# Kernel tuning notes

Measured on AMD Instinct MI355X. Metric: run time of the kernel, lower is better.

## Reference

```python
import jax, jax.numpy as jnp
import numpy as np

N_QUBITS = 64
L = 128
K = 2
B = 4096
M_EVO = 5
A = N_QUBITS * 3 * M_EVO  # 960
E = 2 * (N_QUBITS - 1)    # 126 directed chain edges


def setup_inputs() -> dict:
    key = jax.random.key(0)
    ks = iter(jax.random.split(key, 32))

    def nrm(shape, s=0.05):
        return jax.random.normal(next(ks), shape, dtype=jnp.float32) * s

    # chain edges, both directions: (i,i+1) and (i+1,i)
    src = jnp.asarray(np.concatenate([np.arange(N_QUBITS - 1), np.arange(1, N_QUBITS)]), dtype=jnp.int32)
    tgt = jnp.asarray(np.concatenate([np.arange(1, N_QUBITS), np.arange(N_QUBITS - 1)]), dtype=jnp.int32)
    edge_attr = jnp.full((E, 1), 0.1, dtype=jnp.float32)

    return {
        "z0": jax.random.normal(next(ks), (B, L), dtype=jnp.float32),
        "src": src,
        "tgt": tgt,
        "edge_attr": edge_attr,
        "phiE_W1": nrm((K, 2 * L + 1, L)), "phiE_b1": jnp.zeros((K, L), jnp.float32),
        "phiE_W2": nrm((K, L, L)),          "phiE_b2": jnp.zeros((K, L), jnp.float32),
        "phiN_W1": nrm((K, 2 * L, L)),      "phiN_b1": jnp.zeros((K, L), jnp.float32),
        "phiN_g": jnp.ones((K, L), jnp.float32), "phiN_be": jnp.zeros((K, L), jnp.float32),
        "phiN_W2": nrm((K, L, L)),          "phiN_b2": jnp.zeros((K, L), jnp.float32),
        "sh_W": nrm((L, 2 * L)),            "sh_b": jnp.zeros((2 * L,), jnp.float32),
        "ln_g": jnp.ones((2 * L,), jnp.float32), "ln_b": jnp.zeros((2 * L,), jnp.float32),
        "pol_W": nrm((2 * L, A)),           "pol_b": jnp.zeros((A,), jnp.float32),
        "val_W": nrm((2 * L, 1)),           "val_b": jnp.zeros((1,), jnp.float32),
    }


def _layernorm(x, g, b, eps=1e-5):
    mu = jnp.mean(x, axis=-1, keepdims=True)
    var = jnp.mean(jnp.square(x - mu), axis=-1, keepdims=True)
    return (x - mu) * jax.lax.rsqrt(var + eps) * g + b


def reference(z0, src, tgt, edge_attr,
              phiE_W1, phiE_b1, phiE_W2, phiE_b2,
              phiN_W1, phiN_b1, phiN_g, phiN_be, phiN_W2, phiN_b2,
              sh_W, sh_b, ln_g, ln_b, pol_W, pol_b, val_W, val_b):
    Bc = z0.shape[0]
    n_nodes = N_QUBITS
    # broadcast latent to every node: h [B, N, L]
    h = jnp.broadcast_to(z0[:, None, :], (Bc, n_nodes, L))
    e = jnp.broadcast_to(edge_attr[None, :, :], (Bc, edge_attr.shape[0], 1))

    for k in range(K):  # K=2 fixed message-passing rounds
        hi = h[:, src, :]   # [B, E, L] gather
        hj = h[:, tgt, :]
        inp_e = jnp.concatenate([hi, hj, e], axis=-1)  # [B, E, 2L+1]
        m = jax.nn.relu(inp_e @ phiE_W1[k] + phiE_b1[k]) @ phiE_W2[k] + phiE_b2[k]
        # scatter-add messages back onto source nodes
        m_agg = jnp.zeros_like(h).at[:, src, :].add(m)  # [B, N, L]
        inp_n = jnp.concatenate([h, m_agg], axis=-1)    # [B, N, 2L]
        u = jax.nn.relu(inp_n @ phiN_W1[k] + phiN_b1[k])
        u = _layernorm(u, phiN_g[k], phiN_be[k])  # dropout is identity in eval
        h = u @ phiN_W2[k] + phiN_b2[k] + h       # residual

    z_G = jnp.mean(h, axis=1)  # [B, L] mean pool over qubit nodes

    # policy/value head (Q-head)
    x = jax.nn.relu(z_G @ sh_W + sh_b)
    x = _layernorm(x, ln_g, ln_b)
    logits = x @ pol_W + pol_b        # [B, A]
    V = (x @ val_W + val_b)[:, 0]     # [B]
    return logits, V
```

## Files before the change

kernel.cpp:

```cpp
#include <hip/hip_runtime.h>


#define OUT_V 3932160

typedef float    floatx4 __attribute__((ext_vector_type(4)));
typedef int      intx4   __attribute__((ext_vector_type(4)));
typedef _Float16 f16x8   __attribute__((ext_vector_type(8)));

static __device__ __forceinline__ float bf2f(unsigned short u) {
    union { unsigned int i; float f; } v; v.i = ((unsigned int)u) << 16; return v.f;
}
static __device__ __forceinline__ unsigned short f2bf(float f) {
    union { float ff; unsigned int i; } v; v.ff = f;
    unsigned int r = v.i + 0x7FFFu + ((v.i >> 16) & 1u);
    return (unsigned short)(r >> 16);
}
static __device__ __forceinline__ float ld(const void* p, int i, bool bf) {
    return bf ? bf2f(((const unsigned short*)p)[i]) : ((const float*)p)[i];
}
static __device__ __forceinline__ void st(void* p, long i, float v, bool bf) {
    if (bf) ((unsigned short*)p)[i] = f2bf(v); else ((float*)p)[i] = v;
}
static __device__ __forceinline__ bool detect_bf16(const void* lnG) {
    return (*(const unsigned int*)lnG) != 0x3F800000u;
}

#define OFF_E1S0  0
#define OFF_E1T1A 16384
#define OFF_E1T1B 32768
#define OFF_E2T0  49152
#define OFF_E2T1  65536
#define OFF_N1T0A 81920
#define OFF_N1T0B 98304
#define OFF_N1T1A 114688
#define OFF_N1T1B 131072
#define OFF_N2T0  147456
#define OFF_N2T1  163840
#define OFF_SHT   180224
#define OFF_PVT   212992
#define WS_HALVES 458752
#define WS_BYTES  (WS_HALVES * 2)

struct PrepDesc { int src_sel; int src_base; int src_stride; int sum_delta; int n_w; int dst_base; int dst_stride; };

__device__ const PrepDesc g_pdesc[29] = {
    {0, 0,      128, 16384, 128, 0,      128},
    {0, 32896,  128, 0,     128, 16384,  128},
    {0, 49280,  128, 0,     128, 32768,  128},
    {1, 0,      128, 0,     128, 49152,  128},
    {1, 16384,  128, 0,     128, 65536,  128},
    {2, 0,      128, 0,     128, 81920,  128},
    {2, 16384,  128, 0,     128, 98304,  128},
    {2, 32768,  128, 0,     128, 114688, 128},
    {2, 49152,  128, 0,     128, 131072, 128},
    {3, 0,      128, 0,     128, 147456, 128},
    {3, 16384,  128, 0,     128, 163840, 128},
    {4, 0,      256, 0,     128, 180224, 128},
    {4, 128,    256, 0,     128, 196608, 128},
    {5, 0,      960, 0, 128, 212992, 256},
    {5, 128,    960, 0, 128, 245760, 256},
    {5, 256,    960, 0, 128, 278528, 256},
    {5, 384,    960, 0, 128, 311296, 256},
    {5, 512,    960, 0, 128, 344064, 256},
    {5, 640,    960, 0, 128, 376832, 256},
    {5, 768,    960, 0, 128, 409600, 256},
    {5, 896,    960, 0, 64,  442368, 256},
    {5, 122880, 960, 0, 128, 213120, 256},
    {5, 123008, 960, 0, 128, 245888, 256},
    {5, 123136, 960, 0, 128, 278656, 256},
    {5, 123264, 960, 0, 128, 311424, 256},
    {5, 123392, 960, 0, 128, 344192, 256},
    {5, 123520, 960, 0, 128, 376960, 256},
    {5, 123648, 960, 0, 128, 409728, 256},
    {5, 123776, 960, 0, 64,  442496, 256},
};

extern "C" __global__ __launch_bounds__(256)
void SymQNet_56642028700125_prep(
    const void* eW1, const void* eW2, const void* nW1, const void* nW2,
    const void* shW, const void* polW, const void* lnG, void* wsv)
{
    __shared__ float Tl[32][129];
    const bool bf = detect_bf16(lnG);
    _Float16* ws = (_Float16*)wsv;
    const int tid = threadIdx.x;
    const int chunk = blockIdx.x >> 2, slice = blockIdx.x & 3;
    PrepDesc d = g_pdesc[chunk];
    const int n0 = slice * 32;
    if (n0 >= d.n_w) return;
    const void* src;
    switch (d.src_sel) {
        case 0: src = eW1; break; case 1: src = eW2; break;
        case 2: src = nW1; break; case 3: src = nW2; break;
        case 4: src = shW; break; default: src = polW; break;
    }
    for (int idx = tid; idx < 4096; idx += 256) {
        int k = idx >> 5, nn = idx & 31;
        float v = ld(src, d.src_base + k * d.src_stride + n0 + nn, bf);
        if (d.sum_delta)
            v += ld(src, d.src_base + d.sum_delta + k * d.src_stride + n0 + nn, bf);
        Tl[nn][k] = v;
    }
    __syncthreads();
    for (int idx = tid; idx < 4096; idx += 256) {
        int nn = idx >> 7, k = idx & 127;
        ws[d.dst_base + (n0 + nn) * d.dst_stride + k] = (_Float16)Tl[nn][k];
    }
}

#if defined(__has_builtin)
#if __has_builtin(__builtin_amdgcn_mfma_f32_16x16x32_f16)
#define USE_MFMA_BUILTIN 1
#endif
#endif

#ifdef USE_MFMA_BUILTIN
#define MFMA4(acc, a, b) (acc) = __builtin_amdgcn_mfma_f32_16x16x32_f16((a), (b), (acc), 0, 0, 0)
#else
#define MFMA4(acc, a, b) asm("s_nop 1\n\tv_mfma_f32_16x16x32_f16 %0, %1, %2, %0\n\ts_nop 7\n\ts_nop 7" \
                             : "+v"(acc) : "v"(a), "v"(b))
#endif

struct AF { f16x8 v[4]; };
struct BF { f16x8 v[4]; };

static __device__ __forceinline__ AF loadA(const _Float16* p) {
    AF f;
    f.v[0] = *(const f16x8*)(p +  0); f.v[1] = *(const f16x8*)(p + 32);
    f.v[2] = *(const f16x8*)(p + 64); f.v[3] = *(const f16x8*)(p + 96);
    return f;
}
static __device__ __forceinline__ BF loadB(const _Float16* p) {
    BF f;
    f.v[0] = *(const f16x8*)(p +  0); f.v[1] = *(const f16x8*)(p + 32);
    f.v[2] = *(const f16x8*)(p + 64); f.v[3] = *(const f16x8*)(p + 96);
    return f;
}
static __device__ __forceinline__ floatx4 mm(const AF& a, const BF& b) {
    floatx4 c0 = {0.f, 0.f, 0.f, 0.f}, c1 = {0.f, 0.f, 0.f, 0.f};
    MFMA4(c0, a.v[0], b.v[0]); MFMA4(c1, a.v[1], b.v[1]);
    MFMA4(c0, a.v[2], b.v[2]); MFMA4(c1, a.v[3], b.v[3]);
    return c0 + c1;
}

#define P_EB1E 0
#define P_EB2  256
#define P_NB1  512
#define P_NB2  768
#define P_SHB  1024
#define P_NG   1280
#define P_NBE  1536
#define P_LNG  1792
#define P_LNB  2048
#define P_VALW 2304
#define P_VALB 2560
#define P_SZ   2564

extern "C" __global__ __launch_bounds__(512, 2)
void SymQNet_56642028700125_mfma(
    const void* z0,  const void* eAtt, const void* eW1,
    const void* eB1, const void* eB2,  const void* nB1,
    const void* nG,  const void* nBe,  const void* nB2,
    const void* shB, const void* lnG,  const void* lnB,
    const void* polB, const void* valW, const void* valB,
    const void* wsv, void* out)
{
    __shared__ _Float16 ZB[16][136], M0[16][136], HA[16][136], HB[16][136];
    __shared__ _Float16 U[48][136], MS[48][136], X[16][264];
    __shared__ float PRM[P_SZ];

    const _Float16* ws = (const _Float16*)wsv;
    const int  tid = threadIdx.x;
    const int  wv  = tid >> 6;
    const int  ln  = tid & 63;
    const int  lr  = ln & 15;
    const int  qd  = ln >> 4;
    const int  b0  = blockIdx.x * 16;
    const bool bf  = detect_bf16(lnG);
    const float e0 = ld(eAtt, 0, bf);
    const int  col = wv * 16 + lr;

    intx4 pf = {0, 0, 0, 0};
    {
        const intx4* w4 = (const intx4*)ws;
        int base = ((blockIdx.x >> 3) & 31) * 1792;
        for (int i = tid; i < 1792; i += 512) {
            intx4 v = w4[base + i];
            pf[0] ^= v[0]; pf[1] ^= v[1]; pf[2] ^= v[2]; pf[3] ^= v[3];
        }
    }
    for (int i = tid; i < 256; i += 512) {
        float w = (i < 128) ? ld(eW1, 32768 + i, bf) : ld(eW1, 65664 + (i - 128), bf);
        PRM[P_EB1E + i] = ld(eB1, i, bf) + e0 * w;
        PRM[P_EB2 + i] = ld(eB2, i, bf);
        PRM[P_NB1 + i] = ld(nB1, i, bf);
        PRM[P_NB2 + i] = ld(nB2, i, bf);
        PRM[P_SHB + i] = ld(shB, i, bf);
        PRM[P_NG  + i] = ld(nG,  i, bf);
        PRM[P_NBE + i] = ld(nBe, i, bf);
        PRM[P_LNG + i] = ld(lnG, i, bf);
        PRM[P_LNB + i] = ld(lnB, i, bf);
        PRM[P_VALW + i] = ld(valW, i, bf);
    }
    if (tid == 0) PRM[P_VALB] = ld(valB, 0, bf);
    for (int e = tid; e < 2048; e += 512) {
        int r = e >> 7, c = e & 127;
        ZB[r][c] = (_Float16)ld(z0, (b0 + r) * 128 + c, bf);
    }
    if ((pf[0] ^ pf[1] ^ pf[2] ^ pf[3]) == (int)0xDEADBEEF)
        ((volatile _Float16*)&U[0][0])[0] = (_Float16)0.f;
    __syncthreads();

    floatx4 t1_save;

    {
        BF bE = loadB(ws + OFF_E1S0  + col * 128 + qd * 8);
        BF bN = loadB(ws + OFF_N1T0A + col * 128 + qd * 8);
        AF aZ = loadA(&ZB[lr][qd * 8]);
        floatx4 ce = mm(aZ, bE);
        t1_save = mm(aZ, bN);
        float bias = PRM[P_EB1E + col];
#pragma unroll
        for (int r = 0; r < 4; ++r) {
            float v = ce[r] + bias;
            U[qd * 4 + r][col] = (_Float16)(v > 0.f ? v : 0.f);
        }
    }
    __syncthreads();

    {
        BF bw = loadB(ws + OFF_E2T0 + col * 128 + qd * 8);
        AF aU = loadA(&U[lr][qd * 8]);
        floatx4 acc = mm(aU, bw);
        float bias = PRM[P_EB2 + col];
#pragma unroll
        for (int r = 0; r < 4; ++r) M0[qd * 4 + r][col] = (_Float16)(acc[r] + bias);
    }
    __syncthreads();

    {
        BF bw = loadB(ws + OFF_N1T0B + col * 128 + qd * 8);
        AF aM = loadA(&M0[lr][qd * 8]);
        floatx4 t2 = mm(aM, bw);
        float bias = PRM[P_NB1 + col];
#pragma unroll
        for (int r = 0; r < 4; ++r) {
            float va = t1_save[r] + t2[r] + bias;
            float vb = t1_save[r] + 2.f * t2[r] + bias;
            U[qd * 4 + r][col]      = (_Float16)(va > 0.f ? va : 0.f);
            U[16 + qd * 4 + r][col] = (_Float16)(vb > 0.f ? vb : 0.f);
        }
    }
    __syncthreads();

    {
        int r = tid >> 4, j0 = (tid & 15) * 8;
        float vals[8], s = 0.f, ss = 0.f;
#pragma unroll
        for (int j = 0; j < 8; ++j) { float f = (float)U[r][j0 + j]; vals[j] = f; s += f; ss += f * f; }
        s  += __shfl_xor(s, 1);  s  += __shfl_xor(s, 2);  s  += __shfl_xor(s, 4);  s  += __shfl_xor(s, 8);
        ss += __shfl_xor(ss, 1); ss += __shfl_xor(ss, 2); ss += __shfl_xor(ss, 4); ss += __shfl_xor(ss, 8);
        float mu = s * (1.f / 128.f);
        float var = ss * (1.f / 128.f) - mu * mu; var = var > 0.f ? var : 0.f;
        float rs = 1.f / sqrtf(var + 1e-5f);
#pragma unroll
        for (int j = 0; j < 8; ++j)
            U[r][j0 + j] = (_Float16)((vals[j] - mu) * rs * PRM[P_NG + j0 + j] + PRM[P_NBE + j0 + j]);
    }
    __syncthreads();

    {
        BF bw = loadB(ws + OFF_N2T0 + col * 128 + qd * 8);
        AF a0 = loadA(&U[lr][qd * 8]);
        AF a1 = loadA(&U[16 + lr][qd * 8]);
        floatx4 ca = mm(a0, bw);
        floatx4 cb = mm(a1, bw);
        float bias = PRM[P_NB2 + col];
#pragma unroll
        for (int r = 0; r < 4; ++r) {
            int row = qd * 4 + r;
            float z = (float)ZB[row][col];
            HA[row][col] = (_Float16)(ca[r] + bias + z);
            HB[row][col] = (_Float16)(cb[r] + bias + z);
        }
    }
    __syncthreads();

    {
        BF ba = loadB(ws + OFF_E1T1A + col * 128 + qd * 8);
        BF bb = loadB(ws + OFF_E1T1B + col * 128 + qd * 8);
        AF aA = loadA(&HA[lr][qd * 8]);
        AF aB = loadA(&HB[lr][qd * 8]);
        floatx4 at = mm(aA, ba), bt = mm(aB, ba);
        floatx4 ab = mm(aA, bb), bv = mm(aB, bb);
        float bias = PRM[P_EB1E + 128 + col];
#pragma unroll
        for (int r = 0; r < 4; ++r) {
            int row = qd * 4 + r;
            float vab = at[r] + bv[r] + bias;
            float vba = bt[r] + ab[r] + bias;
            float vbb = bt[r] + bv[r] + bias;
            U[row][col]      = (_Float16)(vab > 0.f ? vab : 0.f);
            U[16 + row][col] = (_Float16)(vba > 0.f ? vba : 0.f);
            U[32 + row][col] = (_Float16)(vbb > 0.f ? vbb : 0.f);
        }
    }
    __syncthreads();

    {
        BF bw = loadB(ws + OFF_E2T1 + col * 128 + qd * 8);
        AF a0 = loadA(&U[lr][qd * 8]);
        AF a1 = loadA(&U[16 + lr][qd * 8]);
        AF a2 = loadA(&U[32 + lr][qd * 8]);
        floatx4 c0 = mm(a0, bw), c1 = mm(a1, bw), c2 = mm(a2, bw);
        float bias = PRM[P_EB2 + 128 + col];
#pragma unroll
        for (int r = 0; r < 4; ++r) {
            int row = qd * 4 + r;
            MS[row][col]      = (_Float16)(c0[r] + bias);
            MS[16 + row][col] = (_Float16)(c1[r] + bias);
            MS[32 + row][col] = (_Float16)(c2[r] + bias);
        }
    }
    __syncthreads();

    {
        BF ba = loadB(ws + OFF_N1T1A + col * 128 + qd * 8);
        BF bb = loadB(ws + OFF_N1T1B + col * 128 + qd * 8);
        AF aA  = loadA(&HA[lr][qd * 8]);
        AF aB  = loadA(&HB[lr][qd * 8]);
        AF am0 = loadA(&MS[lr][qd * 8]);
        AF am1 = loadA(&MS[16 + lr][qd * 8]);
        AF am2 = loadA(&MS[32 + lr][qd * 8]);
        floatx4 hA = mm(aA, ba),  hB = mm(aB, ba);
        floatx4 p0 = mm(am0, bb), p1 = mm(am1, bb), p2 = mm(am2, bb);
        float bias = PRM[P_NB1 + 128 + col];
#pragma unroll
        for (int r = 0; r < 4; ++r) {
            int row = qd * 4 + r;
            float vA = hA[r] + p0[r] + bias;
            float vB = hB[r] + p1[r] + p2[r] + bias;
            float vC = hB[r] + 2.f * p2[r] + bias;
            U[row][col]      = (_Float16)(vA > 0.f ? vA : 0.f);
            U[16 + row][col] = (_Float16)(vB > 0.f ? vB : 0.f);
            U[32 + row][col] = (_Float16)(vC > 0.f ? vC : 0.f);
        }
    }
    __syncthreads();

    {
        int r = tid >> 3, j0 = (tid & 7) * 16;
        if (r < 48) {
            float vals[16], s = 0.f, ss = 0.f;
#pragma unroll
            for (int j = 0; j < 16; ++j) { float f = (float)U[r][j0 + j]; vals[j] = f; s += f; ss += f * f; }
            s  += __shfl_xor(s, 1);  s  += __shfl_xor(s, 2);  s  += __shfl_xor(s, 4);
            ss += __shfl_xor(ss, 1); ss += __shfl_xor(ss, 2); ss += __shfl_xor(ss, 4);
            float mu = s * (1.f / 128.f);
            float var = ss * (1.f / 128.f) - mu * mu; var = var > 0.f ? var : 0.f;
            float rs = 1.f / sqrtf(var + 1e-5f);
#pragma unroll
            for (int j = 0; j < 16; ++j)
                U[r][j0 + j] = (_Float16)((vals[j] - mu) * rs * PRM[P_NG + 128 + j0 + j]
                                          + PRM[P_NBE + 128 + j0 + j]);
        }
    }
    __syncthreads();

    {
        BF bw = loadB(ws + OFF_N2T1 + col * 128 + qd * 8);
        AF a0 = loadA(&U[lr][qd * 8]);
        AF a1 = loadA(&U[16 + lr][qd * 8]);
        AF a2 = loadA(&U[32 + lr][qd * 8]);
        floatx4 c0 = mm(a0, bw), c1 = mm(a1, bw), c2 = mm(a2, bw);
        float bias = PRM[P_NB2 + 128 + col];
#pragma unroll
        for (int r = 0; r < 4; ++r) {
            int row = qd * 4 + r;
            float ra = (float)HA[row][col], rb = (float)HB[row][col];
            float vA = c0[r] + bias + ra;
            float vB = c1[r] + bias + rb;
            float vC = c2[r] + bias + rb;
            ZB[row][col] = (_Float16)((2.f * vA + 2.f * vB + 60.f * vC) * (1.f / 64.f));
        }
    }
    __syncthreads();

    {
        BF b0 = loadB(ws + OFF_SHT + col * 128 + qd * 8);
        BF b1 = loadB(ws + OFF_SHT + (col + 128) * 128 + qd * 8);
        AF aZ = loadA(&ZB[lr][qd * 8]);
        floatx4 c0 = mm(aZ, b0), c1 = mm(aZ, b1);
        float bias0 = PRM[P_SHB + col], bias1 = PRM[P_SHB + col + 128];
#pragma unroll
        for (int r = 0; r < 4; ++r) {
            float v0 = c0[r] + bias0, v1 = c1[r] + bias1;
            X[qd * 4 + r][col]       = (_Float16)(v0 > 0.f ? v0 : 0.f);
            X[qd * 4 + r][col + 128] = (_Float16)(v1 > 0.f ? v1 : 0.f);
        }
    }
    __syncthreads();

    {
        int r = tid >> 5, j0 = (tid & 31) * 8;
        float vals[8], s = 0.f, ss = 0.f;
#pragma unroll
        for (int j = 0; j < 8; ++j) { float f = (float)X[r][j0 + j]; vals[j] = f; s += f; ss += f * f; }
        s  += __shfl_xor(s, 1);  s  += __shfl_xor(s, 2);  s  += __shfl_xor(s, 4);
        s  += __shfl_xor(s, 8);  s  += __shfl_xor(s, 16);
        ss += __shfl_xor(ss, 1); ss += __shfl_xor(ss, 2); ss += __shfl_xor(ss, 4);
        ss += __shfl_xor(ss, 8); ss += __shfl_xor(ss, 16);
        float mu = s * (1.f / 256.f);
        float var = ss * (1.f / 256.f) - mu * mu; var = var > 0.f ? var : 0.f;
        float rs = 1.f / sqrtf(var + 1e-5f);
#pragma unroll
        for (int j = 0; j < 8; ++j)
            X[r][j0 + j] = (_Float16)((vals[j] - mu) * rs * PRM[P_LNG + j0 + j] + PRM[P_LNB + j0 + j]);
    }
    __syncthreads();

    {
        AF aX0 = loadA(&X[lr][qd * 8]);
        AF aX1 = loadA(&X[lr][128 + qd * 8]);
#pragma unroll 2
        for (int t = wv; t < 60; t += 8) {
            int pc = t * 16 + lr;
            BF w0 = loadB(ws + OFF_PVT + pc * 256 + qd * 8);
            BF w1 = loadB(ws + OFF_PVT + pc * 256 + 128 + qd * 8);
            floatx4 acc = mm(aX0, w0) + mm(aX1, w1);
            float bias = ld(polB, pc, bf);
#pragma unroll
            for (int r = 0; r < 4; ++r) {
                long row = b0 + qd * 4 + r;
                st(out, row * 960 + pc, acc[r] + bias, bf);
            }
        }
    }

    {
        int r = tid >> 5, j0 = (tid & 31) * 8;
        float p = 0.f;
#pragma unroll
        for (int j = 0; j < 8; ++j) p += (float)X[r][j0 + j] * PRM[P_VALW + j0 + j];
        p += __shfl_xor(p, 1); p += __shfl_xor(p, 2); p += __shfl_xor(p, 4);
        p += __shfl_xor(p, 8); p += __shfl_xor(p, 16);
        if ((tid & 31) == 0) st(out, OUT_V + b0 + r, p + PRM[P_VALB], bf);
    }
}

extern "C" __global__ __launch_bounds__(256)
void SymQNet_56642028700125_valu(
    const void* z0,  const void* eAtt,
    const void* eW1, const void* eB1, const void* eW2, const void* eB2,
    const void* nW1, const void* nB1, const void* nG,  const void* nBe,
    const void* nW2, const void* nB2,
    const void* shW, const void* shB, const void* lnG, const void* lnB,
    const void* polW, const void* polB, const void* valW, const void* valB,
    void* out)
{
    __shared__ float ZB[8][132], M0[8][132], HA[8][132], HB[8][132];
    __shared__ float U[24][132], MS[24][132];
    __shared__ float X[8][260];

    const int  tid = threadIdx.x;
    const int  b0  = blockIdx.x * 8;
    const bool bf  = detect_bf16(lnG);
    const float e0 = ld(eAtt, 0, bf);
    const int c = tid & 127;
    const int r0 = (tid >> 7) * 4;

    for (int e = tid; e < 1024; e += 256) {
        int r = e >> 7, cc = e & 127;
        ZB[r][cc] = ld(z0, (b0 + r) * 128 + cc, bf);
    }
    __syncthreads();
    {
        float acc[4] = {0.f, 0.f, 0.f, 0.f};
#pragma unroll 4
        for (int k = 0; k < 128; ++k) {
            float w = ld(eW1, k * 128 + c, bf) + ld(eW1, (128 + k) * 128 + c, bf);
#pragma unroll
            for (int j = 0; j < 4; ++j) acc[j] += ZB[r0 + j][k] * w;
        }
        float bias = ld(eB1, c, bf) + e0 * ld(eW1, 256 * 128 + c, bf);
#pragma unroll
        for (int j = 0; j < 4; ++j) { float v = acc[j] + bias; U[r0 + j][c] = v > 0.f ? v : 0.f; }
    }
    __syncthreads();
    {
        float acc[4] = {0.f, 0.f, 0.f, 0.f};
#pragma unroll 4
        for (int k = 0; k < 128; ++k) {
            float w = ld(eW2, k * 128 + c, bf);
#pragma unroll
            for (int j = 0; j < 4; ++j) acc[j] += U[r0 + j][k] * w;
        }
        float bias = ld(eB2, c, bf);
#pragma unroll
        for (int j = 0; j < 4; ++j) M0[r0 + j][c] = acc[j] + bias;
    }
    __syncthreads();
    {
        float t1[4] = {0.f, 0.f, 0.f, 0.f}, t2[4] = {0.f, 0.f, 0.f, 0.f};
#pragma unroll 4
        for (int k = 0; k < 128; ++k) {
            float w1 = ld(nW1, k * 128 + c, bf);
            float w2 = ld(nW1, (128 + k) * 128 + c, bf);
#pragma unroll
            for (int j = 0; j < 4; ++j) { t1[j] += ZB[r0 + j][k] * w1; t2[j] += M0[r0 + j][k] * w2; }
        }
        float bias = ld(nB1, c, bf);
#pragma unroll
        for (int j = 0; j < 4; ++j) {
            float va = t1[j] + t2[j] + bias;       va = va > 0.f ? va : 0.f;
            float vb = t1[j] + 2.f * t2[j] + bias; vb = vb > 0.f ? vb : 0.f;
            U[r0 + j][c] = va; U[8 + r0 + j][c] = vb;
        }
    }
    __syncthreads();
    {
        int r = tid >> 4, j0 = (tid & 15) * 8;
        float vals[8], s = 0.f, ss = 0.f;
#pragma unroll
        for (int j = 0; j < 8; ++j) { float f = U[r][j0 + j]; vals[j] = f; s += f; ss += f * f; }
        s  += __shfl_xor(s, 1);  s  += __shfl_xor(s, 2);  s  += __shfl_xor(s, 4);  s  += __shfl_xor(s, 8);
        ss += __shfl_xor(ss, 1); ss += __shfl_xor(ss, 2); ss += __shfl_xor(ss, 4); ss += __shfl_xor(ss, 8);
        float mu = s * (1.f / 128.f);
        float var = ss * (1.f / 128.f) - mu * mu; var = var > 0.f ? var : 0.f;
        float rs = 1.f / sqrtf(var + 1e-5f);
#pragma unroll
        for (int j = 0; j < 8; ++j)
            U[r][j0 + j] = (vals[j] - mu) * rs * ld(nG, j0 + j, bf) + ld(nBe, j0 + j, bf);
    }
    __syncthreads();
    {
        float a0[4] = {0.f, 0.f, 0.f, 0.f}, a1[4] = {0.f, 0.f, 0.f, 0.f};
#pragma unroll 4
        for (int k = 0; k < 128; ++k) {
            float w = ld(nW2, k * 128 + c, bf);
#pragma unroll
            for (int j = 0; j < 4; ++j) { a0[j] += U[r0 + j][k] * w; a1[j] += U[8 + r0 + j][k] * w; }
        }
        float bias = ld(nB2, c, bf);
#pragma unroll
        for (int j = 0; j < 4; ++j) {
            HA[r0 + j][c] = a0[j] + bias + ZB[r0 + j][c];
            HB[r0 + j][c] = a1[j] + bias + ZB[r0 + j][c];
        }
    }
    __syncthreads();
    {
        float at[4] = {0.f,0.f,0.f,0.f}, bt[4] = {0.f,0.f,0.f,0.f};
        float ab[4] = {0.f,0.f,0.f,0.f}, bb[4] = {0.f,0.f,0.f,0.f};
#pragma unroll 4
        for (int k = 0; k < 128; ++k) {
            float w1 = ld(eW1, 32896 + k * 128 + c, bf);
            float w2 = ld(eW1, 32896 + (128 + k) * 128 + c, bf);
#pragma unroll
            for (int j = 0; j < 4; ++j) {
                float ha = HA[r0 + j][k], hb = HB[r0 + j][k];
                at[j] += ha * w1; bt[j] += hb * w1; ab[j] += ha * w2; bb[j] += hb * w2;
            }
        }
        float bias = ld(eB1, 128 + c, bf) + e0 * ld(eW1, 32896 + 256 * 128 + c, bf);
#pragma unroll
        for (int j = 0; j < 4; ++j) {
            float vab = at[j] + bb[j] + bias; vab = vab > 0.f ? vab : 0.f;
            float vba = bt[j] + ab[j] + bias; vba = vba > 0.f ? vba : 0.f;
            float vbb = bt[j] + bb[j] + bias; vbb = vbb > 0.f ? vbb : 0.f;
            U[r0 + j][c] = vab; U[8 + r0 + j][c] = vba; U[16 + r0 + j][c] = vbb;
        }
    }
    __syncthreads();
    {
        float acc[3][4] = {{0.f,0.f,0.f,0.f},{0.f,0.f,0.f,0.f},{0.f,0.f,0.f,0.f}};
#pragma unroll 4
        for (int k = 0; k < 128; ++k) {
            float w = ld(eW2, 16384 + k * 128 + c, bf);
#pragma unroll
            for (int mt = 0; mt < 3; ++mt)
#pragma unroll
                for (int j = 0; j < 4; ++j) acc[mt][j] += U[mt * 8 + r0 + j][k] * w;
        }
        float bias = ld(eB2, 128 + c, bf);
#pragma unroll
        for (int mt = 0; mt < 3; ++mt)
#pragma unroll
            for (int j = 0; j < 4; ++j) MS[mt * 8 + r0 + j][c] = acc[mt][j] + bias;
    }
    __syncthreads();
    {
        float hA[4]={0.f,0.f,0.f,0.f}, hB[4]={0.f,0.f,0.f,0.f};
        float pab[4]={0.f,0.f,0.f,0.f}, pba[4]={0.f,0.f,0.f,0.f}, pbb[4]={0.f,0.f,0.f,0.f};
#pragma unroll 4
        for (int k = 0; k < 128; ++k) {
            float w1 = ld(nW1, 32768 + k * 128 + c, bf);
            float w2 = ld(nW1, 32768 + (128 + k) * 128 + c, bf);
#pragma unroll
            for (int j = 0; j < 4; ++j) {
                hA[j]  += HA[r0 + j][k] * w1;
                hB[j]  += HB[r0 + j][k] * w1;
                pab[j] += MS[r0 + j][k] * w2;
                pba[j] += MS[8 + r0 + j][k] * w2;
                pbb[j] += MS[16 + r0 + j][k] * w2;
            }
        }
        float bias = ld(nB1, 128 + c, bf);
#pragma unroll
        for (int j = 0; j < 4; ++j) {
            float vA = hA[j] + pab[j] + bias;          vA = vA > 0.f ? vA : 0.f;
            float vB = hB[j] + pba[j] + pbb[j] + bias; vB = vB > 0.f ? vB : 0.f;
            float vC = hB[j] + 2.f * pbb[j] + bias;    vC = vC > 0.f ? vC : 0.f;
            U[r0 + j][c] = vA; U[8 + r0 + j][c] = vB; U[16 + r0 + j][c] = vC;
        }
    }
    __syncthreads();
    {
        int r = tid >> 3, j0 = (tid & 7) * 16;
        if (r < 24) {
            float vals[16], s = 0.f, ss = 0.f;
#pragma unroll
            for (int j = 0; j < 16; ++j) { float f = U[r][j0 + j]; vals[j] = f; s += f; ss += f * f; }
            s  += __shfl_xor(s, 1);  s  += __shfl_xor(s, 2);  s  += __shfl_xor(s, 4);
            ss += __shfl_xor(ss, 1); ss += __shfl_xor(ss, 2); ss += __shfl_xor(ss, 4);
            float mu = s * (1.f / 128.f);
            float var = ss * (1.f / 128.f) - mu * mu; var = var > 0.f ? var : 0.f;
            float rs = 1.f / sqrtf(var + 1e-5f);
#pragma unroll
            for (int j = 0; j < 16; ++j)
                U[r][j0 + j] = (vals[j] - mu) * rs * ld(nG, 128 + j0 + j, bf) + ld(nBe, 128 + j0 + j, bf);
        }
    }
    __syncthreads();
    {
        float acc[3][4] = {{0.f,0.f,0.f,0.f},{0.f,0.f,0.f,0.f},{0.f,0.f,0.f,0.f}};
#pragma unroll 4
        for (int k = 0; k < 128; ++k) {
            float w = ld(nW2, 16384 + k * 128 + c, bf);
#pragma unroll
            for (int mt = 0; mt < 3; ++mt)
#pragma unroll
                for (int j = 0; j < 4; ++j) acc[mt][j] += U[mt * 8 + r0 + j][k] * w;
        }
        float bias = ld(nB2, 128 + c, bf);
#pragma unroll
        for (int j = 0; j < 4; ++j) {
            MS[r0 + j][c]      = acc[0][j] + bias + HA[r0 + j][c];
            MS[8 + r0 + j][c]  = acc[1][j] + bias + HB[r0 + j][c];
            MS[16 + r0 + j][c] = acc[2][j] + bias + HB[r0 + j][c];
        }
    }
    __syncthreads();
    for (int e = tid; e < 1024; e += 256) {
        int r = e >> 7, cc = e & 127;
        ZB[r][cc] = (2.f * MS[r][cc] + 2.f * MS[8 + r][cc] + 60.f * MS[16 + r][cc]) * (1.f / 64.f);
    }
    __syncthreads();
    {
        float acc[8] = {0.f,0.f,0.f,0.f,0.f,0.f,0.f,0.f};
#pragma unroll 4
        for (int k = 0; k < 128; ++k) {
            float w = ld(shW, k * 256 + tid, bf);
#pragma unroll
            for (int r = 0; r < 8; ++r) acc[r] += ZB[r][k] * w;
        }
        float bias = ld(shB, tid, bf);
#pragma unroll
        for (int r = 0; r < 8; ++r) { float v = acc[r] + bias; X[r][tid] = v > 0.f ? v : 0.f; }
    }
    __syncthreads();
    {
        int r = tid >> 5, j0 = (tid & 31) * 8;
        float vals[8], s = 0.f, ss = 0.f;
#pragma unroll
        for (int j = 0; j < 8; ++j) { float f = X[r][j0 + j]; vals[j] = f; s += f; ss += f * f; }
        s  += __shfl_xor(s, 1);  s  += __shfl_xor(s, 2);  s  += __shfl_xor(s, 4);
        s  += __shfl_xor(s, 8);  s  += __shfl_xor(s, 16);
        ss += __shfl_xor(ss, 1); ss += __shfl_xor(ss, 2); ss += __shfl_xor(ss, 4);
        ss += __shfl_xor(ss, 8); ss += __shfl_xor(ss, 16);
        float mu = s * (1.f / 256.f);
        float var = ss * (1.f / 256.f) - mu * mu; var = var > 0.f ? var : 0.f;
        float rs = 1.f / sqrtf(var + 1e-5f);
#pragma unroll
        for (int j = 0; j < 8; ++j)
            X[r][j0 + j] = (vals[j] - mu) * rs * ld(lnG, j0 + j, bf) + ld(lnB, j0 + j, bf);
    }
    __syncthreads();
    {
        float acc[4][8];
#pragma unroll
        for (int s = 0; s < 4; ++s)
#pragma unroll
            for (int r = 0; r < 8; ++r) acc[s][r] = 0.f;
#pragma unroll 2
        for (int k = 0; k < 256; ++k) {
            float xv[8];
#pragma unroll
            for (int r = 0; r < 8; ++r) xv[r] = X[r][k];
#pragma unroll
            for (int s = 0; s < 4; ++s) {
                int col = tid + s * 256;
                if (col < 960) {
                    float w = ld(polW, k * 960 + col, bf);
#pragma unroll
                    for (int r = 0; r < 8; ++r) acc[s][r] += xv[r] * w;
                }
            }
        }
#pragma unroll
        for (int s = 0; s < 4; ++s) {
            int col = tid + s * 256;
            if (col < 960) {
                float bias = ld(polB, col, bf);
#pragma unroll
                for (int r = 0; r < 8; ++r) st(out, (long)(b0 + r) * 960 + col, acc[s][r] + bias, bf);
            }
        }
    }
    {
        int r = tid >> 5, j0 = (tid & 31) * 8;
        float p = 0.f;
#pragma unroll
        for (int j = 0; j < 8; ++j) p += X[r][j0 + j] * ld(valW, j0 + j, bf);
        p += __shfl_xor(p, 1); p += __shfl_xor(p, 2); p += __shfl_xor(p, 4);
        p += __shfl_xor(p, 8); p += __shfl_xor(p, 16);
        if ((tid & 31) == 0) st(out, OUT_V + b0 + r, p + ld(valB, 0, bf), bf);
    }
}

extern "C" void kernel_launch(void* const* d_in, const int* in_sizes, int n_in,
                              void* d_out, int out_size, void* d_ws, size_t ws_size,
                              hipStream_t stream) {
    const void* z0   = d_in[0];
    const void* eAtt = d_in[3];
    const void* eW1  = d_in[4];
    const void* eB1  = d_in[5];
    const void* eW2  = d_in[6];
    const void* eB2  = d_in[7];
    const void* nW1  = d_in[8];
    const void* nB1  = d_in[9];
    const void* nG   = d_in[10];
    const void* nBe  = d_in[11];
    const void* nW2  = d_in[12];
    const void* nB2  = d_in[13];
    const void* shW  = d_in[14];
    const void* shB  = d_in[15];
    const void* lnG  = d_in[16];
    const void* lnB  = d_in[17];
    const void* polW = d_in[18];
    const void* polB = d_in[19];
    const void* valW = d_in[20];
    const void* valB = d_in[21];
    (void)in_sizes; (void)n_in; (void)out_size;

    if (ws_size >= (size_t)WS_BYTES) {
        SymQNet_56642028700125_prep<<<dim3(116), dim3(256), 0, stream>>>(
            eW1, eW2, nW1, nW2, shW, polW, lnG, d_ws);
        SymQNet_56642028700125_mfma<<<dim3(256), dim3(512), 0, stream>>>(
            z0, eAtt, eW1, eB1, eB2, nB1, nG, nBe, nB2, shB, lnG, lnB,
            polB, valW, valB, d_ws, d_out);
    } else {
        SymQNet_56642028700125_valu<<<dim3(512), dim3(256), 0, stream>>>(
            z0, eAtt, eW1, eB1, eW2, eB2, nW1, nB1, nG, nBe, nW2, nB2,
            shW, shB, lnG, lnB, polW, polB, valW, valB, d_out);
    }
}
```

Before: 146.7 us.

## Prefetch per-stage weight fragments into registers ahead of use, drop L2 warm loop

Loads each stage's MFMA B-operand weight fragments into registers one or more stages before they are consumed, so global loads overlap earlier matmuls and barriers. The policy-head loop is software-pipelined to fetch the next tile's weights while computing the current one. The XOR-based L2 warm-up read of the weight workspace is removed. This raises live register count and relies on the hardware cache rather than explicit warming.

```diff
diff --git a/kernel.cpp b/kernel.cpp
--- a/kernel.cpp
+++ b/kernel.cpp
@@ -179,16 +179,14 @@
     const bool bf  = detect_bf16(lnG);
     const float e0 = ld(eAtt, 0, bf);
     const int  col = wv * 16 + lr;
-
-    intx4 pf = {0, 0, 0, 0};
-    {
-        const intx4* w4 = (const intx4*)ws;
-        int base = ((blockIdx.x >> 3) & 31) * 1792;
-        for (int i = tid; i < 1792; i += 512) {
-            intx4 v = w4[base + i];
-            pf[0] ^= v[0]; pf[1] ^= v[1]; pf[2] ^= v[2]; pf[3] ^= v[3];
-        }
-    }
+    const int  boff = col * 128 + qd * 8;
+
+    BF bS1e = loadB(ws + OFF_E1S0  + boff);
+    BF bS1n = loadB(ws + OFF_N1T0A + boff);
+    BF bS2  = loadB(ws + OFF_E2T0  + boff);
+    BF bS3  = loadB(ws + OFF_N1T0B + boff);
+    BF bS4  = loadB(ws + OFF_N2T0  + boff);
+
     for (int i = tid; i < 256; i += 512) {
         float w = (i < 128) ? ld(eW1, 32768 + i, bf) : ld(eW1, 65664 + (i - 128), bf);
         PRM[P_EB1E + i] = ld(eB1, i, bf) + e0 * w;
@@ -207,18 +205,17 @@
         int r = e >> 7, c = e & 127;
         ZB[r][c] = (_Float16)ld(z0, (b0 + r) * 128 + c, bf);
     }
-    if ((pf[0] ^ pf[1] ^ pf[2] ^ pf[3]) == (int)0xDEADBEEF)
-        ((volatile _Float16*)&U[0][0])[0] = (_Float16)0.f;
     __syncthreads();
 
     floatx4 t1_save;
 
-    {
-        BF bE = loadB(ws + OFF_E1S0  + col * 128 + qd * 8);
-        BF bN = loadB(ws + OFF_N1T0A + col * 128 + qd * 8);
+    BF bS5a, bS5b;
+    {
         AF aZ = loadA(&ZB[lr][qd * 8]);
-        floatx4 ce = mm(aZ, bE);
-        t1_save = mm(aZ, bN);
+        floatx4 ce = mm(aZ, bS1e);
+        t1_save = mm(aZ, bS1n);
+        bS5a = loadB(ws + OFF_E1T1A + boff);
+        bS5b = loadB(ws + OFF_E1T1B + boff);
         float bias = PRM[P_EB1E + col];
 #pragma unroll
         for (int r = 0; r < 4; ++r) {
@@ -228,20 +225,22 @@
     }
     __syncthreads();
 
-    {
-        BF bw = loadB(ws + OFF_E2T0 + col * 128 + qd * 8);
+    BF bS6;
+    {
         AF aU = loadA(&U[lr][qd * 8]);
-        floatx4 acc = mm(aU, bw);
+        floatx4 acc = mm(aU, bS2);
+        bS6 = loadB(ws + OFF_E2T1 + boff);
         float bias = PRM[P_EB2 + col];
 #pragma unroll
         for (int r = 0; r < 4; ++r) M0[qd * 4 + r][col] = (_Float16)(acc[r] + bias);
     }
     __syncthreads();
 
-    {
-        BF bw = loadB(ws + OFF_N1T0B + col * 128 + qd * 8);
+    BF bS7a;
+    {
         AF aM = loadA(&M0[lr][qd * 8]);
-        floatx4 t2 = mm(aM, bw);
+        floatx4 t2 = mm(aM, bS3);
+        bS7a = loadB(ws + OFF_N1T1A + boff);
         float bias = PRM[P_NB1 + col];
 #pragma unroll
         for (int r = 0; r < 4; ++r) {
@@ -253,7 +252,9 @@
     }
     __syncthreads();
 
-    {
+    BF bS7b;
+    {
+        bS7b = loadB(ws + OFF_N1T1B + boff);
         int r = tid >> 4, j0 = (tid & 15) * 8;
         float vals[8], s = 0.f, ss = 0.f;
 #pragma unroll
@@ -269,12 +270,13 @@
     }
     __syncthreads();
 
-    {
-        BF bw = loadB(ws + OFF_N2T0 + col * 128 + qd * 8);
+    BF bS8;
+    {
         AF a0 = loadA(&U[lr][qd * 8]);
         AF a1 = loadA(&U[16 + lr][qd * 8]);
-        floatx4 ca = mm(a0, bw);
-        floatx4 cb = mm(a1, bw);
+        floatx4 ca = mm(a0, bS4);
+        floatx4 cb = mm(a1, bS4);
+        bS8 = loadB(ws + OFF_N2T1 + boff);
         float bias = PRM[P_NB2 + col];
 #pragma unroll
         for (int r = 0; r < 4; ++r) {
@@ -286,13 +288,13 @@
     }
     __syncthreads();
 
-    {
-        BF ba = loadB(ws + OFF_E1T1A + col * 128 + qd * 8);
-        BF bb = loadB(ws + OFF_E1T1B + col * 128 + qd * 8);
+    BF bS9a;
+    {
         AF aA = loadA(&HA[lr][qd * 8]);
         AF aB = loadA(&HB[lr][qd * 8]);
-        floatx4 at = mm(aA, ba), bt = mm(aB, ba);
-        floatx4 ab = mm(aA, bb), bv = mm(aB, bb);
+        floatx4 at = mm(aA, bS5a), bt = mm(aB, bS5a);
+        floatx4 ab = mm(aA, bS5b), bv = mm(aB, bS5b);
+        bS9a = loadB(ws + OFF_SHT + boff);
         float bias = PRM[P_EB1E + 128 + col];
 #pragma unroll
         for (int r = 0; r < 4; ++r) {
@@ -307,12 +309,13 @@
     }
     __syncthreads();
 
-    {
-        BF bw = loadB(ws + OFF_E2T1 + col * 128 + qd * 8);
+    BF bS9b;
+    {
         AF a0 = loadA(&U[lr][qd * 8]);
         AF a1 = loadA(&U[16 + lr][qd * 8]);
         AF a2 = loadA(&U[32 + lr][qd * 8]);
-        floatx4 c0 = mm(a0, bw), c1 = mm(a1, bw), c2 = mm(a2, bw);
+        floatx4 c0 = mm(a0, bS6), c1 = mm(a1, bS6), c2 = mm(a2, bS6);
+        bS9b = loadB(ws + OFF_SHT + (col + 128) * 128 + qd * 8);
         float bias = PRM[P_EB2 + 128 + col];
 #pragma unroll
         for (int r = 0; r < 4; ++r) {
@@ -324,16 +327,18 @@
     }
     __syncthreads();
 
-    {
-        BF ba = loadB(ws + OFF_N1T1A + col * 128 + qd * 8);
-        BF bb = loadB(ws + OFF_N1T1B + col * 128 + qd * 8);
+    BF bP0, bP1;
+    {
         AF aA  = loadA(&HA[lr][qd * 8]);
         AF aB  = loadA(&HB[lr][qd * 8]);
         AF am0 = loadA(&MS[lr][qd * 8]);
         AF am1 = loadA(&MS[16 + lr][qd * 8]);
         AF am2 = loadA(&MS[32 + lr][qd * 8]);
-        floatx4 hA = mm(aA, ba),  hB = mm(aB, ba);
-        floatx4 p0 = mm(am0, bb), p1 = mm(am1, bb), p2 = mm(am2, bb);
+        floatx4 hA = mm(aA, bS7a),  hB = mm(aB, bS7a);
+        floatx4 p0 = mm(am0, bS7b), p1 = mm(am1, bS7b), p2 = mm(am2, bS7b);
+        int pc0 = wv * 16 + lr;
+        bP0 = loadB(ws + OFF_PVT + pc0 * 256 + qd * 8);
+        bP1 = loadB(ws + OFF_PVT + pc0 * 256 + 128 + qd * 8);
         float bias = PRM[P_NB1 + 128 + col];
 #pragma unroll
         for (int r = 0; r < 4; ++r) {
@@ -368,11 +373,10 @@
     __syncthreads();
 
     {
-        BF bw = loadB(ws + OFF_N2T1 + col * 128 + qd * 8);
         AF a0 = loadA(&U[lr][qd * 8]);
         AF a1 = loadA(&U[16 + lr][qd * 8]);
         AF a2 = loadA(&U[32 + lr][qd * 8]);
-        floatx4 c0 = mm(a0, bw), c1 = mm(a1, bw), c2 = mm(a2, bw);
+        floatx4 c0 = mm(a0, bS8), c1 = mm(a1, bS8), c2 = mm(a2, bS8);
         float bias = PRM[P_NB2 + 128 + col];
 #pragma unroll
         for (int r = 0; r < 4; ++r) {
@@ -387,10 +391,8 @@
     __syncthreads();
 
     {
-        BF b0 = loadB(ws + OFF_SHT + col * 128 + qd * 8);
-        BF b1 = loadB(ws + OFF_SHT + (col + 128) * 128 + qd * 8);
         AF aZ = loadA(&ZB[lr][qd * 8]);
-        floatx4 c0 = mm(aZ, b0), c1 = mm(aZ, b1);
+        floatx4 c0 = mm(aZ, bS9a), c1 = mm(aZ, bS9b);
         float bias0 = PRM[P_SHB + col], bias1 = PRM[P_SHB + col + 128];
 #pragma unroll
         for (int r = 0; r < 4; ++r) {
@@ -422,11 +424,14 @@
     {
         AF aX0 = loadA(&X[lr][qd * 8]);
         AF aX1 = loadA(&X[lr][128 + qd * 8]);
-#pragma unroll 2
         for (int t = wv; t < 60; t += 8) {
             int pc = t * 16 + lr;
-            BF w0 = loadB(ws + OFF_PVT + pc * 256 + qd * 8);
-            BF w1 = loadB(ws + OFF_PVT + pc * 256 + 128 + qd * 8);
+            BF w0 = bP0, w1 = bP1;
+            int nt = t + 8;
+            if (nt < 60) {
+                bP0 = loadB(ws + OFF_PVT + (nt * 16 + lr) * 256 + qd * 8);
+                bP1 = loadB(ws + OFF_PVT + (nt * 16 + lr) * 256 + 128 + qd * 8);
+            }
             floatx4 acc = mm(aX0, w0) + mm(aX1, w1);
             float bias = ld(polB, pc, bf);
 #pragma unroll
```

Result: faster. 140.2 us (-4.4%).
